# Optimization experiments

Hardware: AMD Instinct MI355X
Metric: run time of the kernel (lower is better)

Reference implementation:

```python
import jax, jax.numpy as jnp
import numpy as np

N_HEADS = 8
N_HEAD_CH = 32
N_GROUPS = 8
NC = N_HEADS * N_HEAD_CH          # 256
GC = NC // N_GROUPS               # 32 group channels
OFFSET_RANGE_FACTOR = 2.0


def _layer_norm(x, w, b, eps=1e-5):
    mu = jnp.mean(x, -1, keepdims=True)
    var = jnp.var(x, -1, keepdims=True)
    return (x - mu) * jax.lax.rsqrt(var + eps) * w + b


def _conv2dmod(x, style, W):
    # StyleGAN2-style modulated 1x1 conv (lucidrains Conv2DMod, demod=True).
    # x (B,Ci,H,W), style (B,Ci), W (Co,Ci)
    w = W[None] * (style[:, None, :] + 1.0)                      # (B,Co,Ci)
    d = jax.lax.rsqrt(jnp.sum(w * w, axis=2, keepdims=True) + 1e-8)
    w = w * d
    return jnp.einsum('boi,bihw->bohw', w, x)


def _dwconv3x3(x, w, b):
    # depthwise 3x3, stride 1, pad 1; w (C,1,3,3)
    out = jax.lax.conv_general_dilated(
        x, w, window_strides=(1, 1), padding=[(1, 1), (1, 1)],
        dimension_numbers=('NCHW', 'OIHW', 'NCHW'),
        feature_group_count=x.shape[1])
    return out + b[None, :, None, None]


def _grid_sample(img, grid):
    # bilinear, align_corners=True, padding_mode='zeros'
    # img (N,C,H,W), grid (N,Hg,Wg,2) in xy order, values in ~[-1,1]
    N, C, H, W = img.shape
    gx = (grid[..., 0] + 1.0) * 0.5 * (W - 1)
    gy = (grid[..., 1] + 1.0) * 0.5 * (H - 1)
    x0 = jnp.floor(gx); y0 = jnp.floor(gy)
    wx1 = gx - x0; wy1 = gy - y0

    def gather(ix, iy):
        valid = ((ix >= 0) & (ix <= W - 1) & (iy >= 0) & (iy <= H - 1)).astype(img.dtype)
        ixc = jnp.clip(ix, 0, W - 1).astype(jnp.int32)
        iyc = jnp.clip(iy, 0, H - 1).astype(jnp.int32)
        vals = jax.vmap(lambda im, yy, xx: im[:, yy, xx])(img, iyc, ixc)  # (N,C,Hg,Wg)
        return vals * valid[:, None]

    x1 = x0 + 1.0; y1 = y0 + 1.0
    return (gather(x0, y0) * ((1 - wx1) * (1 - wy1))[:, None]
            + gather(x1, y0) * (wx1 * (1 - wy1))[:, None]
            + gather(x0, y1) * ((1 - wx1) * wy1)[:, None]
            + gather(x1, y1) * (wx1 * wy1)[:, None])


def _ref_points(Hk, Wk, BG, dtype):
    ry = jnp.linspace(0.5, Hk - 0.5, Hk, dtype=dtype) / (Hk - 1.0) * 2.0 - 1.0
    rx = jnp.linspace(0.5, Wk - 0.5, Wk, dtype=dtype) / (Wk - 1.0) * 2.0 - 1.0
    ref = jnp.stack(jnp.meshgrid(ry, rx, indexing='ij'), -1)  # (Hk,Wk,2) yx
    return jnp.broadcast_to(ref[None], (BG, Hk, Wk, 2))


def setup_inputs() -> dict:
    key = jax.random.key(0)
    ks = jax.random.split(key, 16)
    s = 0.02
    inp = {
        'x': jax.random.normal(ks[0], (2, NC, 32, 32), jnp.float32),
        'q': jax.random.normal(ks[1], (8, 2048, NC), jnp.float32),
        'mask': (jax.random.uniform(ks[2], (8, 2048, 1)) > 0.2).astype(jnp.float32),
        'Wq': jax.random.normal(ks[3], (NC, NC), jnp.float32) * s,
        'bq': jnp.zeros((NC,), jnp.float32),
        'Wmod': jax.random.normal(ks[4], (NC, NC), jnp.float32),
        'dw_w': jax.random.normal(ks[5], (GC, 1, 3, 3), jnp.float32) * s,
        'dw_b': jnp.zeros((GC,), jnp.float32),
        'ln_w': jnp.ones((GC,), jnp.float32),
        'ln_b': jnp.zeros((GC,), jnp.float32),
        'off_w': jax.random.normal(ks[6], (2, GC), jnp.float32) * s,
        'Wk': jax.random.normal(ks[7], (NC, NC), jnp.float32) * s,
        'bk': jnp.zeros((NC,), jnp.float32),
        'Wv': jax.random.normal(ks[8], (NC, NC), jnp.float32) * s,
        'bv': jnp.zeros((NC,), jnp.float32),
        'Wo': jax.random.normal(ks[9], (NC, NC), jnp.float32) * s,
        'bo': jnp.zeros((NC,), jnp.float32),
    }
    return inp


def reference(x, q, mask, Wq, bq, Wmod, dw_w, dw_b, ln_w, ln_b, off_w,
              Wk, bk, Wv, bv, Wo, bo):
    rn = q.shape[0] // x.shape[0]
    B, L, C = q.shape
    H, W = x.shape[2], x.shape[3]

    # masked mean pooling of queries -> conditioning vector
    q_cond = jnp.sum(q * mask, axis=1) / (jnp.sum(mask, axis=1) + 1e-6)   # (B,C)
    q_cond = q_cond @ Wq.T + bq

    # tile reference features: 'ref_n c h w -> (rn ref_n) c h w'
    xr = jnp.tile(x, (rn, 1, 1, 1))                                       # (B,C,H,W)

    # modulated 1x1 conv, then per-group offset network
    q_t = _conv2dmod(xr, q_cond, Wmod)                                    # (B,C,H,W)
    q_off = q_t.reshape(B * N_GROUPS, GC, H, W)
    t = _dwconv3x3(q_off, dw_w, dw_b)
    t = jnp.transpose(t, (0, 2, 3, 1))
    t = _layer_norm(t, ln_w, ln_b)
    t = jax.nn.gelu(t, approximate=False)
    t = jnp.transpose(t, (0, 3, 1, 2))
    offset = jnp.einsum('oi,bihw->bohw', off_w, t)                        # (BG,2,Hk,Wk)

    Hk, Wk_ = offset.shape[2], offset.shape[3]
    n_sample = Hk * Wk_
    offset_range = jnp.array([1.0 / (Hk - 1.0), 1.0 / (Wk_ - 1.0)],
                             dtype=x.dtype).reshape(1, 2, 1, 1)
    offset = jnp.tanh(offset) * offset_range * OFFSET_RANGE_FACTOR
    offset = jnp.transpose(offset, (0, 2, 3, 1))                          # (BG,Hk,Wk,2) yx

    ref = _ref_points(Hk, Wk_, B * N_GROUPS, x.dtype)
    pos = offset + ref                                                    # no clamp (orf>=0)

    # deformable gather
    xs = _grid_sample(xr.reshape(B * N_GROUPS, GC, H, W), pos[..., ::-1]) # (BG,GC,Hk,Wk)
    xs = xs.reshape(B, C, 1, n_sample)

    k = (jnp.einsum('oi,bimn->bomn', Wk, xs) + bk[None, :, None, None]
         ).reshape(B * N_HEADS, N_HEAD_CH, n_sample)
    v = (jnp.einsum('oi,bimn->bomn', Wv, xs) + bv[None, :, None, None]
         ).reshape(B * N_HEADS, N_HEAD_CH, n_sample)
    qh = jnp.transpose(q, (0, 2, 1)).reshape(B * N_HEADS, N_HEAD_CH, L)

    scale = N_HEAD_CH ** (-0.5)
    attn = jnp.einsum('bcm,bcn->bmn', qh, k) * scale                      # (BH,L,ns)
    # NOTE: source's attn.masked_fill(...) is non-in-place and discarded -> no mask here
    attn = jax.nn.softmax(attn, axis=2)
    out = jnp.einsum('bmn,bcn->bcm', attn, v)                             # (BH,hc,L)

    # '(b gn) c l -> b l (gn c)' with gn = n_groups (== n_heads)
    out = out.reshape(B, N_GROUPS, N_HEAD_CH, L).transpose(0, 3, 1, 2).reshape(B, L, NC)
    y = out @ Wo.T + bo
    return (y,
            pos.reshape(B, N_GROUPS, Hk, Wk_, 2),
            ref.reshape(B, N_GROUPS, Hk, Wk_, 2))
```

## Files before the change

kernel.cpp:

```cpp
#include <hip/hip_runtime.h>
#include <math.h>

typedef unsigned int uint;
typedef unsigned short ushort;
typedef __attribute__((ext_vector_type(8))) short short8;
typedef __attribute__((ext_vector_type(4))) float f32x4;

constexpr int CB  = 8;
constexpr int CL  = 2048;
constexpr int CC  = 256;
constexpr int CHC = 32;
constexpr int CGC = 32;
constexpr int CHW = 1024;
constexpr int CNS = 1024;
constexpr int CBG = 64;

constexpr size_t WS_WMOD  = 4224;
constexpr size_t WS_XT    = 266368;
constexpr size_t WS_QT    = 528512;
constexpr size_t WS_XST   = 2756736;
constexpr size_t WS_KB    = 3805312;
constexpr size_t WS_VB    = 4853888;
constexpr size_t WS_WB    = 5902464;
constexpr size_t WS_TMPB  = 6000768;
constexpr size_t WS_QB    = 8097920;
constexpr size_t WS_PART  = 10195072;
constexpr size_t WS_MPART = 10260608;

static __device__ __forceinline__ ushort f2bf(float f) {
  uint u = __float_as_uint(f);
  return (ushort)((u + 0x7FFFu + ((u >> 16) & 1u)) >> 16);
}
static __device__ __forceinline__ float bf2f(ushort u) {
  return __uint_as_float((uint)u << 16);
}
static __device__ __forceinline__ uint pack2bf(float a, float b) {
  return (uint)f2bf(a) | ((uint)f2bf(b) << 16);
}
static __device__ __forceinline__ uint packtrunc(float lo, float hi) {
  return __builtin_amdgcn_perm(__float_as_uint(hi), __float_as_uint(lo), 0x07060302u);
}

__global__ void k_poolprep(const float* __restrict__ q, const float* __restrict__ mask,
                           float* __restrict__ part, float* __restrict__ mpart,
                           ushort* __restrict__ qb,
                           const float* __restrict__ x, const float* __restrict__ Wk,
                           const float* __restrict__ Wv, const float* __restrict__ Wo,
                           ushort* __restrict__ xt, ushort* __restrict__ wb) {
  int bid = blockIdx.x;
  int tid = threadIdx.x;
  __shared__ float shbuf[64 * 65];
  if (bid < 256) {
    int b  = bid >> 5;
    int lc = bid & 31;
    int l0 = lc * 64;
    const float scale = 0.17677669529663687f * 1.4426950408889634f;
    float* mloc = shbuf;
    if (tid < 64) mloc[tid] = mask[b * CL + l0 + tid];
    __syncthreads();
    if (tid == 0) {
      float s = 0.f;
      for (int j = 0; j < 64; j++) s += mloc[j];
      mpart[b * 32 + lc] = s;
    }
    float acc = 0.f;
    const float* qp = q + (size_t)(b * CL + l0) * CC + tid;
    ushort* qw = qb + (size_t)(b * CL + l0) * CC + tid;
    for (int j = 0; j < 64; j++) {
      float v = qp[(size_t)j * CC];
      acc += v * mloc[j];
      qw[(size_t)j * CC] = f2bf(v * scale);
    }
    part[((size_t)(b * 32 + lc)) * CC + tid] = acc;
  } else if (bid < 384) {
    int b2 = bid - 256;
    int ref  = b2 >> 6;
    int cblk = (b2 >> 4) & 3;
    int hwblk = b2 & 15;
    float (*t)[65] = (float(*)[65])shbuf;
    int c0 = cblk * 64, hw0 = hwblk * 64;
    const float* src = x + (size_t)ref * CC * CHW;
    int hl = tid & 63, cq = tid >> 6;
    #pragma unroll
    for (int r = 0; r < 16; r++) {
      int cl = cq * 16 + r;
      t[cl][hl] = src[(size_t)(c0 + cl) * CHW + hw0 + hl];
    }
    __syncthreads();
    int cl2 = tid & 63, hq = tid >> 6;
    #pragma unroll
    for (int r = 0; r < 16; r++) {
      int hwl = hq * 16 + r;
      xt[((size_t)(ref * CHW + hw0 + hwl)) * CC + c0 + cl2] = f2bf(t[cl2][hwl]);
    }
  } else {
    int t2 = (bid - 384) * 256 + tid;
    int which = t2 >> 13;
    size_t off = ((size_t)(t2 & 8191)) * 8;
    const float* src = (which == 0) ? Wk : (which == 1) ? Wv : Wo;
    float4 a = *(const float4*)(src + off);
    float4 b = *(const float4*)(src + off + 4);
    uint4 r;
    r.x = pack2bf(a.x, a.y); r.y = pack2bf(a.z, a.w);
    r.z = pack2bf(b.x, b.y); r.w = pack2bf(b.z, b.w);
    *(uint4*)(wb + (size_t)which * 65536 + off) = r;
  }
}

__global__ void k_wprep(const float* __restrict__ part, const float* __restrict__ mpart,
                        const float* __restrict__ Wq, const float* __restrict__ bq,
                        const float* __restrict__ Wmod, ushort* __restrict__ wmodb) {
  int b  = blockIdx.x >> 4;
  int og = blockIdx.x & 15;
  int tid = threadIdx.x;
  __shared__ float qm[CC];
  __shared__ float qcond_s[CC];
  __shared__ float msh;

  float s = 0.f;
  const float* pp = part + (size_t)b * 32 * CC + tid;
  #pragma unroll
  for (int lc = 0; lc < 32; lc++) s += pp[(size_t)lc * CC];
  if (tid < 32) {
    float m = mpart[b * 32 + tid];
    #pragma unroll
    for (int k = 1; k < 32; k <<= 1) m += __shfl_xor(m, k, 32);
    if (tid == 0) msh = m;
  }
  __syncthreads();
  qm[tid] = s * (1.f / (msh + 1e-6f));
  __syncthreads();
  float qc = bq[tid];
  const float* wrow = Wq + (size_t)tid * CC;
  for (int i = 0; i < CC; i++) qc += wrow[i] * qm[i];
  qcond_s[tid] = qc;
  __syncthreads();

  int ol = tid >> 4, seg = tid & 15;
  int o = og * 16 + ol;
  const float* wr = Wmod + (size_t)o * CC + seg * 16;
  float m[16];
  float ss = 0.f;
  #pragma unroll
  for (int j = 0; j < 16; j++) {
    float v = wr[j] * (qcond_s[seg * 16 + j] + 1.f);
    m[j] = v;
    ss += v * v;
  }
  #pragma unroll
  for (int k = 1; k < 16; k <<= 1) ss += __shfl_xor(ss, k, 16);
  float d = rsqrtf(ss + 1e-8f);
  uint u[8];
  #pragma unroll
  for (int j = 0; j < 8; j++) u[j] = pack2bf(m[2 * j] * d, m[2 * j + 1] * d);
  ushort* dst = wmodb + ((size_t)(b * CC + o)) * CC + seg * 16;
  *(uint4*)(dst)     = make_uint4(u[0], u[1], u[2], u[3]);
  *(uint4*)(dst + 8) = make_uint4(u[4], u[5], u[6], u[7]);
}

__launch_bounds__(256)
__global__ void k_mod_mfma(const ushort* __restrict__ wmodb, const ushort* __restrict__ xt,
                           ushort* __restrict__ qtb) {
  int tid = threadIdx.x;
  int wid = tid >> 6, lane = tid & 63;
  int widx = blockIdx.x * 4 + wid;
  int b   = widx >> 8;
  int og  = (widx >> 5) & 7;
  int hg  = widx & 31;
  int col = lane & 15, g = lane >> 4;
  int O0 = og * 32, HW0 = hg * 32;
  const ushort* ap0 = wmodb + ((size_t)(b * CC + O0 + col)) * CC + g * 8;
  const ushort* ap1 = ap0 + (size_t)16 * CC;
  const ushort* bp0 = xt + ((size_t)((b & 1) * CHW + HW0 + col)) * CC + g * 8;
  const ushort* bp1 = bp0 + (size_t)16 * CC;
  f32x4 acc[2][2];
  #pragma unroll
  for (int X = 0; X < 2; X++)
    #pragma unroll
    for (int Y = 0; Y < 2; Y++)
      acc[X][Y] = (f32x4){0.f, 0.f, 0.f, 0.f};
  #pragma unroll
  for (int ks = 0; ks < 8; ks++) {
    short8 af0 = *(const short8*)(ap0 + ks * 32);
    short8 af1 = *(const short8*)(ap1 + ks * 32);
    short8 bf0 = *(const short8*)(bp0 + ks * 32);
    short8 bf1 = *(const short8*)(bp1 + ks * 32);
    acc[0][0] = __builtin_amdgcn_mfma_f32_16x16x32_bf16(af0, bf0, acc[0][0], 0, 0, 0);
    acc[0][1] = __builtin_amdgcn_mfma_f32_16x16x32_bf16(af0, bf1, acc[0][1], 0, 0, 0);
    acc[1][0] = __builtin_amdgcn_mfma_f32_16x16x32_bf16(af1, bf0, acc[1][0], 0, 0, 0);
    acc[1][1] = __builtin_amdgcn_mfma_f32_16x16x32_bf16(af1, bf1, acc[1][1], 0, 0, 0);
  }
  #pragma unroll
  for (int X = 0; X < 2; X++)
    #pragma unroll
    for (int Y = 0; Y < 2; Y++) {
      uint2 st;
      st.x = pack2bf(acc[X][Y][0], acc[X][Y][1]);
      st.y = pack2bf(acc[X][Y][2], acc[X][Y][3]);
      *(uint2*)(qtb + ((size_t)(b * CHW + HW0 + Y * 16 + col)) * CC + O0 + X * 16 + g * 4) = st;
    }
}

__global__ void k_off_sample(const ushort* __restrict__ qtb, const float* __restrict__ dww,
                             const float* __restrict__ dwb, const float* __restrict__ lnw,
                             const float* __restrict__ lnb, const float* __restrict__ offw,
                             const ushort* __restrict__ xt,
                             float* __restrict__ out_pos, float* __restrict__ out_ref,
                             ushort* __restrict__ xst) {
  int bg   = blockIdx.x >> 7;
  int pblk = blockIdx.x & 127;
  int tid  = threadIdx.x;
  int c = tid & 31, pp = tid >> 5;
  int p0 = pblk * 8;
  int yy = p0 >> 5;
  int xx = (p0 & 31) + pp;
  int p  = p0 + pp;
  const ushort* src = qtb + ((size_t)(bg >> 3) * CHW) * CC + (bg & 7) * CGC + c;
  float acc = dwb[c];
  #pragma unroll
  for (int ky = 0; ky < 3; ky++) {
    int yr = yy + ky - 1;
    if (yr < 0 || yr > 31) continue;
    #pragma unroll
    for (int kx = 0; kx < 3; kx++) {
      int xc = xx + kx - 1;
      if (xc < 0 || xc > 31) continue;
      acc += dww[c * 9 + ky * 3 + kx] * bf2f(src[(size_t)(yr * 32 + xc) * CC]);
    }
  }
  float s1 = acc, s2 = acc * acc;
  #pragma unroll
  for (int m = 1; m < 32; m <<= 1) { s1 += __shfl_xor(s1, m, 32); s2 += __shfl_xor(s2, m, 32); }
  float mu  = s1 * (1.f / 32.f);
  float var = s2 * (1.f / 32.f) - mu * mu;
  float tn  = (acc - mu) * rsqrtf(var + 1e-5f) * lnw[c] + lnb[c];
  float g   = 0.5f * tn * (1.f + erff(tn * 0.70710678118654752f));
  float sy = offw[c] * g, sx = offw[32 + c] * g;
  #pragma unroll
  for (int m = 1; m < 32; m <<= 1) { sy += __shfl_xor(sy, m, 32); sx += __shfl_xor(sx, m, 32); }

  float mine  = tanhf((c & 1) ? sx : sy);
  float other = __shfl_xor(mine, 1, 32);
  float ty = (c & 1) ? other : mine;
  float tx = (c & 1) ? mine : other;

  float refy = (0.5f + (float)yy) * (2.f / 31.f) - 1.f;
  float refx = (0.5f + (float)xx) * (2.f / 31.f) - 1.f;
  float py = ty * (2.f / 31.f) + refy;
  float px = tx * (2.f / 31.f) + refx;
  if (c < 2) {
    int oidx = bg * 2048 + p * 2 + c;
    out_pos[oidx] = (c == 0) ? py : px;
    out_ref[oidx] = (c == 0) ? refy : refx;
  }

  float gx = (px + 1.f) * 15.5f;
  float gy = (py + 1.f) * 15.5f;
  float x0f = floorf(gx), y0f = floorf(gy);
  float wx = gx - x0f, wy = gy - y0f;
  int ix0 = (int)x0f, iy0 = (int)y0f;
  const ushort* img = xt + (size_t)(((bg >> 3) & 1)) * CHW * CC + (bg & 7) * CGC + c;
  float sacc = 0.f;
  #pragma unroll
  for (int dy = 0; dy < 2; dy++) {
    int iy = iy0 + dy;
    if (iy < 0 || iy > 31) continue;
    float wyv = dy ? wy : 1.f - wy;
    #pragma unroll
    for (int dx = 0; dx < 2; dx++) {
      int ix = ix0 + dx;
      if (ix < 0 || ix > 31) continue;
      float wxv = dx ? wx : 1.f - wx;
      sacc += wyv * wxv * bf2f(img[(size_t)(iy * 32 + ix) * CC]);
    }
  }
  xst[((size_t)((bg >> 3) * CNS) + p) * CC + (bg & 7) * CGC + c] = f2bf(sacc);
}

__launch_bounds__(256)
__global__ void k_kv_mfma(const ushort* __restrict__ xst, const ushort* __restrict__ wkb,
                          const ushort* __restrict__ wvb, const float* __restrict__ bk,
                          const float* __restrict__ bv, ushort* __restrict__ kb,
                          ushort* __restrict__ vb) {
  int tid = threadIdx.x;
  int wid = tid >> 6, lane = tid & 63;
  int widx = blockIdx.x * 4 + wid;
  int b   = widx >> 8;
  int ntg = (widx >> 3) & 31;
  int otg = widx & 7;
  int col = lane & 15, g = lane >> 4;
  int N0 = ntg * 32, O0 = otg * 32;

  const ushort* xs0 = xst + ((size_t)(b * CNS + N0 + col)) * CC + g * 8;
  const ushort* xs1 = xs0 + (size_t)16 * CC;
  const ushort* wk0 = wkb + (size_t)(O0 + col) * CC + g * 8;
  const ushort* wk1 = wk0 + (size_t)16 * CC;
  const ushort* wv0 = wvb + (size_t)(O0 + col) * CC + g * 8;
  const ushort* wv1 = wv0 + (size_t)16 * CC;

  f32x4 ka[2][2], va[2][2];
  #pragma unroll
  for (int Y = 0; Y < 2; Y++) {
    float bvv = bv[O0 + Y * 16 + col];
    #pragma unroll
    for (int r = 0; r < 4; r++) {
      float bkv = bk[O0 + Y * 16 + g * 4 + r];
      ka[0][Y][r] = bkv; ka[1][Y][r] = bkv;
      va[0][Y][r] = bvv; va[1][Y][r] = bvv;
    }
  }

  #pragma unroll
  for (int ks = 0; ks < 8; ks++) {
    short8 xf0 = *(const short8*)(xs0 + ks * 32);
    short8 xf1 = *(const short8*)(xs1 + ks * 32);
    short8 kf0 = *(const short8*)(wk0 + ks * 32);
    short8 kf1 = *(const short8*)(wk1 + ks * 32);
    short8 vf0 = *(const short8*)(wv0 + ks * 32);
    short8 vf1 = *(const short8*)(wv1 + ks * 32);
    ka[0][0] = __builtin_amdgcn_mfma_f32_16x16x32_bf16(kf0, xf0, ka[0][0], 0, 0, 0);
    ka[0][1] = __builtin_amdgcn_mfma_f32_16x16x32_bf16(kf1, xf0, ka[0][1], 0, 0, 0);
    ka[1][0] = __builtin_amdgcn_mfma_f32_16x16x32_bf16(kf0, xf1, ka[1][0], 0, 0, 0);
    ka[1][1] = __builtin_amdgcn_mfma_f32_16x16x32_bf16(kf1, xf1, ka[1][1], 0, 0, 0);
    va[0][0] = __builtin_amdgcn_mfma_f32_16x16x32_bf16(xf0, vf0, va[0][0], 0, 0, 0);
    va[0][1] = __builtin_amdgcn_mfma_f32_16x16x32_bf16(xf0, vf1, va[0][1], 0, 0, 0);
    va[1][0] = __builtin_amdgcn_mfma_f32_16x16x32_bf16(xf1, vf0, va[1][0], 0, 0, 0);
    va[1][1] = __builtin_amdgcn_mfma_f32_16x16x32_bf16(xf1, vf1, va[1][1], 0, 0, 0);
  }

  #pragma unroll
  for (int X = 0; X < 2; X++)
    #pragma unroll
    for (int Y = 0; Y < 2; Y++) {
      int Oy = O0 + Y * 16, Nx = N0 + X * 16;
      {
        int hh = Oy >> 5;
        int c0 = (Oy & 31) + g * 4;
        uint2 w;
        w.x = pack2bf(ka[X][Y][0], ka[X][Y][1]);
        w.y = pack2bf(ka[X][Y][2], ka[X][Y][3]);
        *(uint2*)(kb + ((size_t)((b * 8 + hh) * CNS + Nx + col)) * CHC + c0) = w;
      }
      {
        int o = Oy + col;
        int hh = o >> 5;
        uint2 w;
        w.x = pack2bf(va[X][Y][0], va[X][Y][1]);
        w.y = pack2bf(va[X][Y][2], va[X][Y][3]);
        *(uint2*)(vb + ((size_t)((b * 8 + hh) * CHC + (o & 31))) * CNS + Nx + g * 4) = w;
      }
    }
}

__launch_bounds__(512, 4)
__global__ void k_attn_mfma(const ushort* __restrict__ qb, const ushort* __restrict__ kb,
                            const ushort* __restrict__ vb, ushort* __restrict__ tmpb) {
  int bh = blockIdx.x >> 3;
  int mb = blockIdx.x & 7;
  int b = bh >> 3, h = bh & 7;
  int tid = threadIdx.x;
  int wid = tid >> 6, lane = tid & 63;
  int col = lane & 15, g = lane >> 4;
  int mA = mb * 256 + wid * 32 + col;

  __shared__ ushort Kst[2][2][64 * 40];
  __shared__ ushort Vst[2][2][32 * 72];
  __shared__ ushort plds[8][2048];

  char* pwA = (char*)&plds[wid][0];
  char* pwB = (char*)&plds[wid][1024];
  int swz = (col & 7) << 4;
  int wb0 = col * 128 + g * 8;
  int rb0 = (col * 128 + g * 16) ^ swz;
  int rb1 = (col * 128 + 64 + g * 16) ^ swz;

  const ushort* qpA = qb + ((size_t)(b * CL + mA)) * CC + h * CHC + g * 8;
  short8 qfA = *(const short8*)qpA;
  short8 qfB = *(const short8*)(qpA + 16 * CC);

  const ushort* kglob = kb + (size_t)bh * 32768 + tid * 4;
  const ushort* vglob = vb + (size_t)bh * 32768 + (tid >> 4) * 1024 + (tid & 15) * 4;
  int kdst = (tid >> 3) * 40 + (tid & 7) * 4;
  int vdst = (tid >> 4) * 72 + (tid & 15) * 4;

  f32x4 oA0 = {0.f,0.f,0.f,0.f}, oA1 = {0.f,0.f,0.f,0.f};
  f32x4 oB0 = {0.f,0.f,0.f,0.f}, oB1 = {0.f,0.f,0.f,0.f};
  float lA = 0.f, lB = 0.f;

  {
    uint2 k0 = *(const uint2*)(kglob);
    uint2 k1 = *(const uint2*)(kglob + 2048);
    uint2 v0 = *(const uint2*)(vglob);
    uint2 v1 = *(const uint2*)(vglob + 64);
    *(uint2*)&Kst[0][0][kdst] = k0;
    *(uint2*)&Kst[0][1][kdst] = k1;
    *(uint2*)&Vst[0][0][vdst] = v0;
    *(uint2*)&Vst[0][1][vdst] = v1;
  }
  __syncthreads();

  int cur = 0;
  for (int it = 0; it < 8; it++) {
    uint2 kx0, kx1, vx0, vx1;
    if (it < 7) {
      int cb = (it + 1) * 2;
      kx0 = *(const uint2*)(kglob + (size_t)cb * 2048);
      kx1 = *(const uint2*)(kglob + (size_t)(cb + 1) * 2048);
      vx0 = *(const uint2*)(vglob + (size_t)cb * 64);
      vx1 = *(const uint2*)(vglob + (size_t)(cb + 1) * 64);
    }

    #pragma unroll
    for (int s = 0; s < 2; s++) {
      const ushort* Kc = &Kst[cur][s][0];
      const ushort* Vc = &Vst[cur][s][0];
      short8 kf0 = *(const short8*)(Kc + ( 0 + col) * 40 + g * 8);
      short8 kf1 = *(const short8*)(Kc + (16 + col) * 40 + g * 8);
      short8 kf2 = *(const short8*)(Kc + (32 + col) * 40 + g * 8);
      short8 kf3 = *(const short8*)(Kc + (48 + col) * 40 + g * 8);
      short8 vf00 = *(const short8*)(Vc + (col     ) * 72 +  0 + g * 8);
      short8 vf01 = *(const short8*)(Vc + (col     ) * 72 + 32 + g * 8);
      short8 vf10 = *(const short8*)(Vc + (col + 16) * 72 +  0 + g * 8);
      short8 vf11 = *(const short8*)(Vc + (col + 16) * 72 + 32 + g * 8);

      f32x4 zero = {0.f,0.f,0.f,0.f};
      f32x4 sA0 = __builtin_amdgcn_mfma_f32_16x16x32_bf16(kf0, qfA, zero, 0, 0, 0);
      f32x4 sA1 = __builtin_amdgcn_mfma_f32_16x16x32_bf16(kf1, qfA, zero, 0, 0, 0);
      f32x4 sA2 = __builtin_amdgcn_mfma_f32_16x16x32_bf16(kf2, qfA, zero, 0, 0, 0);
      f32x4 sA3 = __builtin_amdgcn_mfma_f32_16x16x32_bf16(kf3, qfA, zero, 0, 0, 0);
      f32x4 sB0 = __builtin_amdgcn_mfma_f32_16x16x32_bf16(kf0, qfB, zero, 0, 0, 0);
      f32x4 sB1 = __builtin_amdgcn_mfma_f32_16x16x32_bf16(kf1, qfB, zero, 0, 0, 0);
      f32x4 sB2 = __builtin_amdgcn_mfma_f32_16x16x32_bf16(kf2, qfB, zero, 0, 0, 0);
      f32x4 sB3 = __builtin_amdgcn_mfma_f32_16x16x32_bf16(kf3, qfB, zero, 0, 0, 0);

      {
        float ps = 0.f;
        #pragma unroll
        for (int f = 0; f < 4; f++) {
          f32x4 sv = (f == 0) ? sA0 : (f == 1) ? sA1 : (f == 2) ? sA2 : sA3;
          float p0 = __builtin_amdgcn_exp2f(sv[0]);
          float p1 = __builtin_amdgcn_exp2f(sv[1]);
          float p2 = __builtin_amdgcn_exp2f(sv[2]);
          float p3 = __builtin_amdgcn_exp2f(sv[3]);
          ps += (p0 + p1) + (p2 + p3);
          *(uint2*)(pwA + ((wb0 + f * 32) ^ swz)) = make_uint2(packtrunc(p0, p1), packtrunc(p2, p3));
        }
        lA += ps;
      }
      {
        float ps = 0.f;
        #pragma unroll
        for (int f = 0; f < 4; f++) {
          f32x4 sv = (f == 0) ? sB0 : (f == 1) ? sB1 : (f == 2) ? sB2 : sB3;
          float p0 = __builtin_amdgcn_exp2f(sv[0]);
          float p1 = __builtin_amdgcn_exp2f(sv[1]);
          float p2 = __builtin_amdgcn_exp2f(sv[2]);
          float p3 = __builtin_amdgcn_exp2f(sv[3]);
          ps += (p0 + p1) + (p2 + p3);
          *(uint2*)(pwB + ((wb0 + f * 32) ^ swz)) = make_uint2(packtrunc(p0, p1), packtrunc(p2, p3));
        }
        lB += ps;
      }

      short8 pfA0 = *(const short8*)(pwA + rb0);
      short8 pfA1 = *(const short8*)(pwA + rb1);
      short8 pfB0 = *(const short8*)(pwB + rb0);
      short8 pfB1 = *(const short8*)(pwB + rb1);

      oA0 = __builtin_amdgcn_mfma_f32_16x16x32_bf16(vf00, pfA0, oA0, 0, 0, 0);
      oA0 = __builtin_amdgcn_mfma_f32_16x16x32_bf16(vf01, pfA1, oA0, 0, 0, 0);
      oA1 = __builtin_amdgcn_mfma_f32_16x16x32_bf16(vf10, pfA0, oA1, 0, 0, 0);
      oA1 = __builtin_amdgcn_mfma_f32_16x16x32_bf16(vf11, pfA1, oA1, 0, 0, 0);
      oB0 = __builtin_amdgcn_mfma_f32_16x16x32_bf16(vf00, pfB0, oB0, 0, 0, 0);
      oB0 = __builtin_amdgcn_mfma_f32_16x16x32_bf16(vf01, pfB1, oB0, 0, 0, 0);
      oB1 = __builtin_amdgcn_mfma_f32_16x16x32_bf16(vf10, pfB0, oB1, 0, 0, 0);
      oB1 = __builtin_amdgcn_mfma_f32_16x16x32_bf16(vf11, pfB1, oB1, 0, 0, 0);
    }

    if (it < 7) {
      *(uint2*)&Kst[cur ^ 1][0][kdst] = kx0;
      *(uint2*)&Kst[cur ^ 1][1][kdst] = kx1;
      *(uint2*)&Vst[cur ^ 1][0][vdst] = vx0;
      *(uint2*)&Vst[cur ^ 1][1][vdst] = vx1;
    }
    __syncthreads();
    cur ^= 1;
  }

  lA += __shfl_xor(lA, 16); lA += __shfl_xor(lA, 32);
  lB += __shfl_xor(lB, 16); lB += __shfl_xor(lB, 32);
  float rlA = 1.f / lA, rlB = 1.f / lB;

  ushort* opA = tmpb + ((size_t)(b * CL + mA)) * CC + h * CHC;
  ushort* opB = opA + 16 * CC;
  {
    uint2 w0, w1;
    w0.x = pack2bf(oA0[0] * rlA, oA0[1] * rlA);
    w0.y = pack2bf(oA0[2] * rlA, oA0[3] * rlA);
    w1.x = pack2bf(oA1[0] * rlA, oA1[1] * rlA);
    w1.y = pack2bf(oA1[2] * rlA, oA1[3] * rlA);
    *(uint2*)(opA + g * 4) = w0;
    *(uint2*)(opA + 16 + g * 4) = w1;
  }
  {
    uint2 w0, w1;
    w0.x = pack2bf(oB0[0] * rlB, oB0[1] * rlB);
    w0.y = pack2bf(oB0[2] * rlB, oB0[3] * rlB);
    w1.x = pack2bf(oB1[0] * rlB, oB1[1] * rlB);
    w1.y = pack2bf(oB1[2] * rlB, oB1[3] * rlB);
    *(uint2*)(opB + g * 4) = w0;
    *(uint2*)(opB + 16 + g * 4) = w1;
  }
}

__launch_bounds__(256)
__global__ void k_yproj_mfma(const ushort* __restrict__ tmpb, const ushort* __restrict__ wob,
                             const float* __restrict__ bo, float* __restrict__ y) {
  int tid = threadIdx.x;
  int wid = tid >> 6, lane = tid & 63;
  int widx = blockIdx.x * 4 + wid;
  int rt2 = widx >> 1;
  int og = widx & 1;
  int col = lane & 15, g = lane >> 4;
  int R0 = rt2 * 32, O0 = og * 128;

  const ushort* ap0 = tmpb + ((size_t)(R0 + col)) * CC + g * 8;
  const ushort* ap1 = ap0 + (size_t)16 * CC;
  const ushort* bp = wob + (size_t)(O0 + col) * CC + g * 8;

  f32x4 acc[2][8];
  #pragma unroll
  for (int o4 = 0; o4 < 8; o4++) {
    float bb = bo[O0 + o4 * 16 + col];
    #pragma unroll
    for (int r = 0; r < 4; r++) { acc[0][o4][r] = bb; acc[1][o4][r] = bb; }
  }

  #pragma unroll
  for (int ks = 0; ks < 8; ks++) {
    short8 af0 = *(const short8*)(ap0 + ks * 32);
    short8 af1 = *(const short8*)(ap1 + ks * 32);
    #pragma unroll
    for (int o4 = 0; o4 < 8; o4++) {
      short8 bf = *(const short8*)(bp + (size_t)o4 * 16 * CC + ks * 32);
      acc[0][o4] = __builtin_amdgcn_mfma_f32_16x16x32_bf16(af0, bf, acc[0][o4], 0, 0, 0);
      acc[1][o4] = __builtin_amdgcn_mfma_f32_16x16x32_bf16(af1, bf, acc[1][o4], 0, 0, 0);
    }
  }

  #pragma unroll
  for (int rr = 0; rr < 2; rr++)
    #pragma unroll
    for (int o4 = 0; o4 < 8; o4++)
      #pragma unroll
      for (int r = 0; r < 4; r++)
        y[(size_t)(R0 + rr * 16 + g * 4 + r) * CC + O0 + o4 * 16 + col] = acc[rr][o4][r];
}

extern "C" void kernel_launch(void* const* d_in, const int* in_sizes, int n_in,
                              void* d_out, int out_size, void* d_ws, size_t ws_size,
                              hipStream_t stream) {
  const float* x    = (const float*)d_in[0];
  const float* q    = (const float*)d_in[1];
  const float* mask = (const float*)d_in[2];
  const float* Wq   = (const float*)d_in[3];
  const float* bq   = (const float*)d_in[4];
  const float* Wmod = (const float*)d_in[5];
  const float* dw_w = (const float*)d_in[6];
  const float* dw_b = (const float*)d_in[7];
  const float* ln_w = (const float*)d_in[8];
  const float* ln_b = (const float*)d_in[9];
  const float* offw = (const float*)d_in[10];
  const float* Wk   = (const float*)d_in[11];
  const float* bk   = (const float*)d_in[12];
  const float* Wv   = (const float*)d_in[13];
  const float* bv   = (const float*)d_in[14];
  const float* Wo   = (const float*)d_in[15];
  const float* bo   = (const float*)d_in[16];

  float* ws = (float*)d_ws;
  float* out = (float*)d_out;
  float* out_y   = out;
  float* out_pos = out + (size_t)CB * CL * CC;
  float* out_ref = out_pos + (size_t)CBG * CHW * 2;

  ushort* wmodb = (ushort*)(ws + WS_WMOD);
  ushort* xt    = (ushort*)(ws + WS_XT);
  ushort* qtb   = (ushort*)(ws + WS_QT);
  ushort* xst   = (ushort*)(ws + WS_XST);
  ushort* kbuf  = (ushort*)(ws + WS_KB);
  ushort* vbuf  = (ushort*)(ws + WS_VB);
  ushort* wkb   = (ushort*)(ws + WS_WB);
  ushort* wvb   = wkb + 65536;
  ushort* wob   = wkb + 131072;
  ushort* tmpb  = (ushort*)(ws + WS_TMPB);
  ushort* qbuf  = (ushort*)(ws + WS_QB);
  float*  part  = ws + WS_PART;
  float*  mpart = ws + WS_MPART;

  k_poolprep<<<480, 256, 0, stream>>>(q, mask, part, mpart, qbuf, x, Wk, Wv, Wo, xt, wkb);
  k_wprep<<<128, 256, 0, stream>>>(part, mpart, Wq, bq, Wmod, wmodb);
  k_mod_mfma<<<512, 256, 0, stream>>>(wmodb, xt, qtb);
  k_off_sample<<<8192, 256, 0, stream>>>(qtb, dw_w, dw_b, ln_w, ln_b, offw, xt,
                                         out_pos, out_ref, xst);
  k_kv_mfma<<<512, 256, 0, stream>>>(xst, wkb, wvb, bk, bv, kbuf, vbuf);
  k_attn_mfma<<<512, 512, 0, stream>>>(qbuf, kbuf, vbuf, tmpb);
  k_yproj_mfma<<<256, 256, 0, stream>>>(tmpb, wob, bo, out_y);
}
```

Before: 118.7 us.

## Fuse weight-modulation prep into mod GEMM and widen attention K/V staging loads

Removes the separate k_wprep launch by having each k_mod_mfma block recompute the pooled query conditioning and its 32-row slice of the demodulated weights directly into shared memory, which saves a kernel launch and the global round trip of wmodb. In exchange, every one of the 512 blocks redundantly runs the 256x256 Wq matvec (previously done by 128 blocks), adding extra serial work per block. Separately, the attention kernel's K/V tile staging switches from two 8-byte loads per thread to one 16-byte load per thread, with threads split across the two sub-slots.

```diff
diff --git a/kernel.cpp b/kernel.cpp
--- a/kernel.cpp
+++ b/kernel.cpp
@@ -15,7 +15,6 @@
 constexpr int CNS = 1024;
 constexpr int CBG = 64;
 
-constexpr size_t WS_WMOD  = 4224;
 constexpr size_t WS_XT    = 266368;
 constexpr size_t WS_QT    = 528512;
 constexpr size_t WS_XST   = 2756736;
@@ -107,70 +106,78 @@
   }
 }
 
-__global__ void k_wprep(const float* __restrict__ part, const float* __restrict__ mpart,
-                        const float* __restrict__ Wq, const float* __restrict__ bq,
-                        const float* __restrict__ Wmod, ushort* __restrict__ wmodb) {
-  int b  = blockIdx.x >> 4;
-  int og = blockIdx.x & 15;
-  int tid = threadIdx.x;
-  __shared__ float qm[CC];
-  __shared__ float qcond_s[CC];
-  __shared__ float msh;
-
-  float s = 0.f;
-  const float* pp = part + (size_t)b * 32 * CC + tid;
-  #pragma unroll
-  for (int lc = 0; lc < 32; lc++) s += pp[(size_t)lc * CC];
-  if (tid < 32) {
-    float m = mpart[b * 32 + tid];
-    #pragma unroll
-    for (int k = 1; k < 32; k <<= 1) m += __shfl_xor(m, k, 32);
-    if (tid == 0) msh = m;
-  }
-  __syncthreads();
-  qm[tid] = s * (1.f / (msh + 1e-6f));
-  __syncthreads();
-  float qc = bq[tid];
-  const float* wrow = Wq + (size_t)tid * CC;
-  for (int i = 0; i < CC; i++) qc += wrow[i] * qm[i];
-  qcond_s[tid] = qc;
-  __syncthreads();
-
-  int ol = tid >> 4, seg = tid & 15;
-  int o = og * 16 + ol;
-  const float* wr = Wmod + (size_t)o * CC + seg * 16;
-  float m[16];
-  float ss = 0.f;
-  #pragma unroll
-  for (int j = 0; j < 16; j++) {
-    float v = wr[j] * (qcond_s[seg * 16 + j] + 1.f);
-    m[j] = v;
-    ss += v * v;
-  }
-  #pragma unroll
-  for (int k = 1; k < 16; k <<= 1) ss += __shfl_xor(ss, k, 16);
-  float d = rsqrtf(ss + 1e-8f);
-  uint u[8];
-  #pragma unroll
-  for (int j = 0; j < 8; j++) u[j] = pack2bf(m[2 * j] * d, m[2 * j + 1] * d);
-  ushort* dst = wmodb + ((size_t)(b * CC + o)) * CC + seg * 16;
-  *(uint4*)(dst)     = make_uint4(u[0], u[1], u[2], u[3]);
-  *(uint4*)(dst + 8) = make_uint4(u[4], u[5], u[6], u[7]);
-}
-
 __launch_bounds__(256)
-__global__ void k_mod_mfma(const ushort* __restrict__ wmodb, const ushort* __restrict__ xt,
+__global__ void k_mod_mfma(const float* __restrict__ part, const float* __restrict__ mpart,
+                           const float* __restrict__ Wq, const float* __restrict__ bq,
+                           const float* __restrict__ Wmod, const ushort* __restrict__ xt,
                            ushort* __restrict__ qtb) {
   int tid = threadIdx.x;
+  int bid = blockIdx.x;
+  int b   = bid >> 6;
+  int og  = (bid >> 3) & 7;
+  int O0  = og * 32;
+
+  __shared__ float qm[CC];
+  __shared__ float qcs[CC];
+  __shared__ float msh;
+  __shared__ ushort wsh[32 * 264];
+
+  {
+    float s = 0.f;
+    const float* pp = part + (size_t)b * 32 * CC + tid;
+    #pragma unroll
+    for (int lc = 0; lc < 32; lc++) s += pp[(size_t)lc * CC];
+    if (tid < 32) {
+      float m = mpart[b * 32 + tid];
+      #pragma unroll
+      for (int k = 1; k < 32; k <<= 1) m += __shfl_xor(m, k, 32);
+      if (tid == 0) msh = m;
+    }
+    __syncthreads();
+    qm[tid] = s * (1.f / (msh + 1e-6f));
+    __syncthreads();
+    float qc = bq[tid];
+    const float* wrow = Wq + (size_t)tid * CC;
+    for (int i = 0; i < CC; i++) qc += wrow[i] * qm[i];
+    qcs[tid] = qc;
+    __syncthreads();
+  }
+
+  {
+    int ol = tid >> 3, seg = tid & 7;
+    int o = O0 + ol;
+    const float* wr = Wmod + (size_t)o * CC + seg * 32;
+    const float* qc = qcs + seg * 32;
+    float m[32];
+    float ss = 0.f;
+    #pragma unroll
+    for (int j = 0; j < 32; j++) {
+      float v = wr[j] * (qc[j] + 1.f);
+      m[j] = v;
+      ss += v * v;
+    }
+    #pragma unroll
+    for (int k = 1; k < 8; k <<= 1) ss += __shfl_xor(ss, k, 8);
+    float d = rsqrtf(ss + 1e-8f);
+    ushort* dst = wsh + ol * 264 + seg * 32;
+    #pragma unroll
+    for (int j4 = 0; j4 < 4; j4++) {
+      uint4 r;
+      r.x = pack2bf(m[j4*8+0]*d, m[j4*8+1]*d);
+      r.y = pack2bf(m[j4*8+2]*d, m[j4*8+3]*d);
+      r.z = pack2bf(m[j4*8+4]*d, m[j4*8+5]*d);
+      r.w = pack2bf(m[j4*8+6]*d, m[j4*8+7]*d);
+      *(uint4*)(dst + j4 * 8) = r;
+    }
+  }
+  __syncthreads();
+
   int wid = tid >> 6, lane = tid & 63;
-  int widx = blockIdx.x * 4 + wid;
-  int b   = widx >> 8;
-  int og  = (widx >> 5) & 7;
-  int hg  = widx & 31;
   int col = lane & 15, g = lane >> 4;
-  int O0 = og * 32, HW0 = hg * 32;
-  const ushort* ap0 = wmodb + ((size_t)(b * CC + O0 + col)) * CC + g * 8;
-  const ushort* ap1 = ap0 + (size_t)16 * CC;
+  int hg = ((bid & 7) << 2) + wid;
+  int HW0 = hg * 32;
+  const ushort* ap0 = wsh + (col) * 264 + g * 8;
+  const ushort* ap1 = wsh + (16 + col) * 264 + g * 8;
   const ushort* bp0 = xt + ((size_t)((b & 1) * CHW + HW0 + col)) * CC + g * 8;
   const ushort* bp1 = bp0 + (size_t)16 * CC;
   f32x4 acc[2][2];
@@ -378,36 +385,30 @@
   short8 qfA = *(const short8*)qpA;
   short8 qfB = *(const short8*)(qpA + 16 * CC);
 
-  const ushort* kglob = kb + (size_t)bh * 32768 + tid * 4;
-  const ushort* vglob = vb + (size_t)bh * 32768 + (tid >> 4) * 1024 + (tid & 15) * 4;
-  int kdst = (tid >> 3) * 40 + (tid & 7) * 4;
-  int vdst = (tid >> 4) * 72 + (tid & 15) * 4;
+  int t2 = tid & 255, slot0 = tid >> 8;
+  const ushort* kglob = kb + (size_t)bh * 32768 + slot0 * 2048 + t2 * 8;
+  const ushort* vglob = vb + (size_t)bh * 32768 + (t2 >> 3) * 1024 + slot0 * 64 + (t2 & 7) * 8;
+  int kdst = (t2 >> 2) * 40 + (t2 & 3) * 8;
+  int vdst = (t2 >> 3) * 72 + (t2 & 7) * 8;
 
   f32x4 oA0 = {0.f,0.f,0.f,0.f}, oA1 = {0.f,0.f,0.f,0.f};
   f32x4 oB0 = {0.f,0.f,0.f,0.f}, oB1 = {0.f,0.f,0.f,0.f};
   float lA = 0.f, lB = 0.f;
 
   {
-    uint2 k0 = *(const uint2*)(kglob);
-    uint2 k1 = *(const uint2*)(kglob + 2048);
-    uint2 v0 = *(const uint2*)(vglob);
-    uint2 v1 = *(const uint2*)(vglob + 64);
-    *(uint2*)&Kst[0][0][kdst] = k0;
-    *(uint2*)&Kst[0][1][kdst] = k1;
-    *(uint2*)&Vst[0][0][vdst] = v0;
-    *(uint2*)&Vst[0][1][vdst] = v1;
+    uint4 kx = *(const uint4*)(kglob);
+    uint4 vx = *(const uint4*)(vglob);
+    *(uint4*)&Kst[0][slot0][kdst] = kx;
+    *(uint4*)&Vst[0][slot0][vdst] = vx;
   }
   __syncthreads();
 
   int cur = 0;
   for (int it = 0; it < 8; it++) {
-    uint2 kx0, kx1, vx0, vx1;
+    uint4 kx, vx;
     if (it < 7) {
-      int cb = (it + 1) * 2;
-      kx0 = *(const uint2*)(kglob + (size_t)cb * 2048);
-      kx1 = *(const uint2*)(kglob + (size_t)(cb + 1) * 2048);
-      vx0 = *(const uint2*)(vglob + (size_t)cb * 64);
-      vx1 = *(const uint2*)(vglob + (size_t)(cb + 1) * 64);
+      kx = *(const uint4*)(kglob + (size_t)(it + 1) * 4096);
+      vx = *(const uint4*)(vglob + (size_t)(it + 1) * 128);
     }
 
     #pragma unroll
@@ -478,10 +479,8 @@
     }
 
     if (it < 7) {
-      *(uint2*)&Kst[cur ^ 1][0][kdst] = kx0;
-      *(uint2*)&Kst[cur ^ 1][1][kdst] = kx1;
-      *(uint2*)&Vst[cur ^ 1][0][vdst] = vx0;
-      *(uint2*)&Vst[cur ^ 1][1][vdst] = vx1;
+      *(uint4*)&Kst[cur ^ 1][slot0][kdst] = kx;
+      *(uint4*)&Vst[cur ^ 1][slot0][vdst] = vx;
     }
     __syncthreads();
     cur ^= 1;
@@ -584,7 +583,6 @@
   float* out_pos = out + (size_t)CB * CL * CC;
   float* out_ref = out_pos + (size_t)CBG * CHW * 2;
 
-  ushort* wmodb = (ushort*)(ws + WS_WMOD);
   ushort* xt    = (ushort*)(ws + WS_XT);
   ushort* qtb   = (ushort*)(ws + WS_QT);
   ushort* xst   = (ushort*)(ws + WS_XST);
@@ -599,8 +597,7 @@
   float*  mpart = ws + WS_MPART;
 
   k_poolprep<<<480, 256, 0, stream>>>(q, mask, part, mpart, qbuf, x, Wk, Wv, Wo, xt, wkb);
-  k_wprep<<<128, 256, 0, stream>>>(part, mpart, Wq, bq, Wmod, wmodb);
-  k_mod_mfma<<<512, 256, 0, stream>>>(wmodb, xt, qtb);
+  k_mod_mfma<<<512, 256, 0, stream>>>(part, mpart, Wq, bq, Wmod, xt, qtb);
   k_off_sample<<<8192, 256, 0, stream>>>(qtb, dw_w, dw_b, ln_w, ln_b, offw, xt,
                                          out_pos, out_ref, xst);
   k_kv_mfma<<<512, 256, 0, stream>>>(xst, wkb, wvb, bk, bv, kbuf, vbuf);
```

After: 124.6 us. +5.0%, slower.
